# Kernel optimization log

Hardware: AMD Instinct MI355X
Metric: run time of the kernel (lower is better)

## Reference

```python
import jax, jax.numpy as jnp
import numpy as np

B, T, C, L = 256, 1024, 128, 64
BLANK = C - 1          # tf.compat.v1.nn.ctc_loss uses num_classes-1 as blank
EPS = 1e-7             # keras.backend.epsilon()
NEG = -1e30            # log-space 'zero'
S = 2 * L + 1          # extended label length (blanks interleaved)


def setup_inputs() -> dict:
    key = jax.random.key(0)
    k1, k2 = jax.random.split(key)
    # y_pred are softmax probabilities (the layer takes log(y_pred + eps))
    y_pred = jax.nn.softmax(jax.random.normal(k1, (B, T, C), dtype=jnp.float32), axis=-1)
    # labels in [0, C-2]; blank (C-1) never appears in targets
    y_true = jax.random.randint(k2, (B, L), 0, C - 1, dtype=jnp.int32)
    return {"y_true": y_true, "y_pred": y_pred}


def _ctc_loss(y_true, y_pred):
    logp = jnp.log(y_pred + EPS)                                   # [B,T,C]
    # extended label sequence: blank, l1, blank, l2, ..., blank -> [B,S]
    ext = jnp.full((B, S), BLANK, dtype=jnp.int32).at[:, 1::2].set(y_true)
    # gather per-extended-symbol log-probs: lp_ext[b,t,s] = logp[b,t,ext[b,s]]
    lp_ext = jnp.take_along_axis(logp[:, :, None, :], ext[:, None, :, None], axis=-1)[..., 0]  # [B,T,S]
    lp_ext = jnp.transpose(lp_ext, (1, 0, 2))                      # [T,B,S] time-major for scan
    # skip transition allowed where ext[s] != blank and ext[s] != ext[s-2]
    can_skip = jnp.concatenate(
        [jnp.zeros((B, 2), dtype=bool), (ext[:, 2:] != BLANK) & (ext[:, 2:] != ext[:, :-2])],
        axis=1)                                                    # [B,S]

    def shift(a, n):
        return jnp.concatenate([jnp.full((B, n), NEG, a.dtype), a[:, : S - n]], axis=1)

    # alpha init at t=0: only s=0 (blank) and s=1 (first label) reachable
    alpha0 = (jnp.full((B, S), NEG)
              .at[:, 0].set(lp_ext[0, :, 0])
              .at[:, 1].set(lp_ext[0, :, 1]))

    def step(alpha, lp_t):
        s1 = shift(alpha, 1)
        s2 = jnp.where(can_skip, shift(alpha, 2), NEG)
        m = jnp.maximum(alpha, jnp.maximum(s1, s2))                # stable log-sum-exp of 3 terms
        new = m + jnp.log(jnp.exp(alpha - m) + jnp.exp(s1 - m) + jnp.exp(s2 - m)) + lp_t
        return new, None

    alphaT, _ = jax.lax.scan(step, alpha0, lp_ext[1:])
    log_lik = jnp.logaddexp(alphaT[:, -1], alphaT[:, -2])          # end in last blank or last label
    return (-log_lik)[:, None]                                     # [B,1], matches expand_dims(..., 1)


def reference(y_true, y_pred):
    return _ctc_loss(y_true, y_pred)
```

## Files before the change

### kernel.cpp

```cpp
#include <hip/hip_runtime.h>


#define B_     256
#define T_     1024
#define C_     128
#define L_     64
#define BLANK_ 127
#define LN2_   0.69314718055994530942f
#define ROWS   32
#define LDSF   (ROWS * C_)
#define XOFF   (6 * LDSF)

__device__ __forceinline__ float flog2(float x) { return __builtin_amdgcn_logf(x); }

template <int CTRL>
__device__ __forceinline__ int dpp_i(int x) {
    return __builtin_amdgcn_update_dpp(x, x, CTRL, 0xF, 0xF, false);
}
__device__ __forceinline__ float ror1_f(float x) {
    return __int_as_float(dpp_i<0x13C>(__float_as_int(x)));
}
__device__ __forceinline__ int ror1_i(int x) { return dpp_i<0x13C>(x); }

__device__ __forceinline__ float fldexp(float x, int n) {
#if __has_builtin(__builtin_amdgcn_ldexpf)
    return __builtin_amdgcn_ldexpf(x, n);
#else
    return ldexpf(x, n);
#endif
}
__device__ __forceinline__ int fexp_of(float x) {
#if __has_builtin(__builtin_amdgcn_frexp_expf)
    return __builtin_amdgcn_frexp_expf(x);
#else
    const int bx = (__float_as_int(x) >> 23) & 0xFF;
    return (x > 0.0f) ? (bx - 126) : 0;
#endif
}

typedef const __attribute__((address_space(1))) void gas_void;
typedef __attribute__((address_space(3))) void las_void;
__device__ __forceinline__ void g2l16(const float* g, float* l) {
    __builtin_amdgcn_global_load_lds((gas_void*)g, (las_void*)l, 16, 0, 0);
}

#define ALSTEP(pL, pB)                                                        \
    {                                                                         \
        const int   ep  = ror1_i(e);                                          \
        const float mpO = ror1_f(aO);                                         \
        const bool dead = (fmaxf(aE, aO) == 0.0f);                            \
        e = dead ? ep : e;                                                    \
        const int   dd  = ep - e;                                             \
        float prevO = fldexp(mpO, dd);                                        \
        prevO = isL0 ? 0.0f : prevO;                                          \
        const float sk = can_skip ? prevO : 0.0f;                             \
        const float nE = (aE + prevO) * (pB);                                 \
        const float nO = (aO + aE + sk) * (pL);                               \
        aZ = (aZ + aO) * (pB);                                                \
        aE = nE; aO = nO;                                                     \
    }

#define RENORM4                                                               \
    {                                                                         \
        const int x = fexp_of(fmaxf(aE, aO));                                 \
        aE = fldexp(aE, -x); aO = fldexp(aO, -x); aZ = fldexp(aZ, -x);        \
        e += x;                                                               \
    }

#define DCALC                                                                 \
    {                                                                         \
        const int ep = ror1_i(e);                                             \
        d = isL0 ? (-16384) : (ep - e);                                       \
    }

#define RENORM4B { RENORM4 DCALC }

#define BLSTEP(pL, pB)                                                        \
    {                                                                         \
        const float prevO = fldexp(ror1_f(aO), d);                            \
        const float nE = (aE + prevO) * (pB);                                 \
        const float nO = __builtin_fmaf(skf, prevO, aO + aE) * (pL);          \
        aZ = (aZ + aO) * (pB);                                                \
        aE = nE; aO = nO;                                                     \
    }

#define ACHUNK(RL, RB)                                                        \
    {                                                                         \
        _Pragma("unroll")                                                     \
        for (int k = 0; k < 32; ++k) {                                        \
            ALSTEP(RL[k], RB[k])                                              \
            if ((k & 3) == 3) RENORM4                                         \
        }                                                                     \
    }

#define BCHUNK32(RL, RB)                                                      \
    {                                                                         \
        _Pragma("unroll")                                                     \
        for (int k = 0; k < 32; ++k) {                                        \
            BLSTEP(RL[k], RB[k])                                              \
            if ((k & 3) == 3) RENORM4B                                        \
        }                                                                     \
    }

#define STAGE16(ROW, LOFF)                                                    \
    {                                                                         \
        const float* src = base + (size_t)(ROW) * C_;                         \
        _Pragma("unroll")                                                     \
        for (int j = 0; j < 16; ++j)                                          \
            g2l16(src + j * 256 + lane * 4, sm + (LOFF) + j * 256);           \
    }

#define FBURSTM(LOFF, RL, RB)                                                 \
    {                                                                         \
        const float* pl = &sm[(LOFF) + lab];                                  \
        const float* pb = &sm[(LOFF) + BLANK_];                               \
        _Pragma("unroll")                                                     \
        for (int j = 0; j < 32; ++j) RL[j] = pl[j * C_];                      \
        _Pragma("unroll")                                                     \
        for (int j = 0; j < 32; ++j) RB[j] = pb[j * C_];                      \
    }
#define RBURSTM(LOFF, RL, RB)                                                 \
    {                                                                         \
        const float* pl = &sm[(LOFF) + lab];                                  \
        const float* pb = &sm[(LOFF) + BLANK_];                               \
        _Pragma("unroll")                                                     \
        for (int j = 0; j < 32; ++j) RL[j] = pl[(31 - j) * C_];               \
        _Pragma("unroll")                                                     \
        for (int j = 0; j < 32; ++j) RB[j] = pb[(31 - j) * C_];               \
    }

#define VMWAIT asm volatile("s_waitcnt vmcnt(0)" ::: "memory")

#define RUN_HALF(SB, CHUNKROW, BURSTM)                                        \
    {                                                                         \
        float rl0[32], rb0[32], rl1[32], rb1[32];                             \
        STAGE16(CHUNKROW(0), (SB))                                            \
        STAGE16(CHUNKROW(1), (SB) + LDSF)                                     \
        aE = isL0 ? ibase[BLANK_] : 0.0f;                                     \
        aO = isL0 ? ibase[lab]    : 0.0f;                                     \
        VMWAIT;                                                               \
        BURSTM((SB), rl0, rb0)                                   \
        STAGE16(CHUNKROW(2), (SB) + 2 * LDSF)                                 \
        BURSTM((SB) + LDSF, rl1, rb1)                            \
        ACHUNK(rl0, rb0)                                                      \
        VMWAIT;                                                               \
        STAGE16(CHUNKROW(3), (SB))                                            \
        BURSTM((SB) + 2 * LDSF, rl0, rb0)                        \
        ACHUNK(rl1, rb1)                                                      \
        VMWAIT;                                                               \
        STAGE16(CHUNKROW(4), (SB) + LDSF)                                     \
        BURSTM((SB), rl1, rb1)                                   \
        ACHUNK(rl0, rb0)                                                      \
        VMWAIT;                                                               \
        STAGE16(CHUNKROW(5), (SB) + 2 * LDSF)                                 \
        BURSTM((SB) + LDSF, rl0, rb0)                            \
        ACHUNK(rl1, rb1)                                                      \
        VMWAIT;                                                               \
        DCALC                                                                 \
        _Pragma("unroll 1")                                                   \
        for (int c = 4; c <= 12; c += 2) {                                    \
            STAGE16(CHUNKROW(c + 2), (SB) + ((c + 2) % 3) * LDSF)             \
            BURSTM((SB) + ((c + 1) % 3) * LDSF, rl1, rb1)                     \
            BCHUNK32(rl0, rb0)                                                \
            VMWAIT;                                                           \
            STAGE16(CHUNKROW(c + 3), (SB) + ((c + 3) % 3) * LDSF)             \
            BURSTM((SB) + ((c + 2) % 3) * LDSF, rl0, rb0)                     \
            BCHUNK32(rl1, rb1)                                                \
            VMWAIT;                                                           \
        }                                                                     \
        BURSTM((SB), rl1, rb1)                          \
        BCHUNK32(rl0, rb0)                                      \
        _Pragma("unroll")                                                     \
        for (int k = 0; k < 31; ++k) {                \
            BLSTEP(rl1[k], rb1[k])                                            \
            if ((k & 3) == 3) RENORM4B                                        \
        }                                                                     \
    }

#define FROW(k) (1 + 32 * (k))
#define RROW(k) (991 - 32 * (k))

#define ACCP(t, Et)                                                           \
    {                                                                         \
        const float t_ = (t); const int Et_ = (Et);                           \
        const int Em = (Eacc > Et_) ? Eacc : Et_;                             \
        acc = fldexp(acc, Eacc - Em) + fldexp(t_, Et_ - Em);                  \
        Eacc = Em;                                                            \
    }

__global__ __launch_bounds__(128, 1)
void ctc_fwd(const int* __restrict__ yt, const float* __restrict__ yp,
             float* __restrict__ out) {
    __shared__ float sm[6 * LDSF + 320];

    const int b    = blockIdx.x;
    const int tid  = threadIdx.x;
    const int wid  = tid >> 6;
    const int lane = tid & 63;
    const int lidx = (wid == 0) ? lane : (63 - lane);
    const int lab  = yt[b * L_ + lidx];
    const int labp = __shfl_up(lab, 1);
    const bool can_skip = (lane > 0) && (lab != labp);
    const bool isL0     = (lane == 0);
    const bool isL63    = (lane == 63);
    const float skf     = can_skip ? 1.0f : 0.0f;

    const float* __restrict__ base  = yp + (size_t)b * T_ * C_;
    const float* __restrict__ ibase = (wid == 0) ? base : (base + 1023 * C_);

    float aE = 0.0f, aO = 0.0f, aZ = 0.0f;
    int   e  = 0, d = 0;

    if (wid == 0) {
        RUN_HALF(0, FROW, FBURSTM)
    } else {
        RUN_HALF(3 * LDSF, RROW, RBURSTM)
        sm[XOFF + lane]        = aE;
        sm[XOFF + 64 + lane]   = aO;
        sm[XOFF + 128 + lane]  = __int_as_float(e);
        sm[XOFF + 192 + lane]  = aZ;
    }

    __syncthreads();

    if (wid == 0) {
        const int i = lane;
        const float rE_hi = isL0 ? sm[XOFF + 192 + 63] : sm[XOFF + 64 - i];
        const int   e_hi  = __float_as_int(isL0 ? sm[XOFF + 128 + 63]
                                                : sm[XOFF + 128 + 64 - i]);
        const float rO_hi = sm[XOFF + 64 + 63 - i];
        const int   eo_hi = __float_as_int(sm[XOFF + 128 + 63 - i]);
        const float rE_nx = isL63 ? sm[XOFF] : sm[XOFF + 63 - i];
        const int   e_nx  = __float_as_int(isL63 ? sm[XOFF + 128]
                                                 : sm[XOFF + 128 + 63 - i]);
        const float rO_nx = isL63 ? 0.0f : sm[XOFF + 64 + 62 - i];
        const int   eo_nx = isL63 ? 0 : __float_as_int(sm[XOFF + 128 + 62 - i]);
        const int   labn  = __shfl_down(lab, 1);
        const float sknE  = (!isL63 && labn != lab) ? 1.0f : 0.0f;

        float acc = aE * rE_hi;
        int  Eacc = e + e_hi;
        ACCP((aE + aO) * rO_hi, e + eo_hi)
        ACCP((isL63 ? (aO + aZ) : aO) * rE_nx, e + e_nx)
        ACCP(sknE * (aO * rO_nx), e + eo_nx)
        if (acc == 0.0f) Eacc = -(1 << 29);

#pragma unroll
        for (int off = 1; off < 64; off <<= 1) {
            const float s2 = __shfl_xor(acc, off);
            const int   E2 = __shfl_xor(Eacc, off);
            const int   Em = (Eacc > E2) ? Eacc : E2;
            acc = fldexp(acc, Eacc - Em) + fldexp(s2, E2 - Em);
            Eacc = Em;
        }
        if (tid == 0) out[b] = -(flog2(acc) + (float)Eacc) * LN2_;
    }
}

extern "C" void kernel_launch(void* const* d_in, const int* in_sizes, int n_in,
                              void* d_out, int out_size, void* d_ws, size_t ws_size,
                              hipStream_t stream) {
    const int*   y_true = (const int*)d_in[0];
    const float* y_pred = (const float*)d_in[1];
    float*       out    = (float*)d_out;
    ctc_fwd<<<B_, 128, 0, stream>>>(y_true, y_pred, out);
}
```

Baseline: 195.5 us.

## Split forward/backward halves into separate single-wave blocks with a meet kernel

```diff
diff --git a/kernel.cpp b/kernel.cpp
--- a/kernel.cpp
+++ b/kernel.cpp
@@ -9,7 +9,6 @@
 #define LN2_   0.69314718055994530942f
 #define ROWS   32
 #define LDSF   (ROWS * C_)
-#define XOFF   (6 * LDSF)
 
 __device__ __forceinline__ float flog2(float x) { return __builtin_amdgcn_logf(x); }
 
@@ -131,44 +130,44 @@
 
 #define VMWAIT asm volatile("s_waitcnt vmcnt(0)" ::: "memory")
 
-#define RUN_HALF(SB, CHUNKROW, BURSTM)                                        \
+#define RUN_HALF(CHUNKROW, BURSTM)                                            \
     {                                                                         \
         float rl0[32], rb0[32], rl1[32], rb1[32];                             \
-        STAGE16(CHUNKROW(0), (SB))                                            \
-        STAGE16(CHUNKROW(1), (SB) + LDSF)                                     \
+        STAGE16(CHUNKROW(0), 0)                                               \
+        STAGE16(CHUNKROW(1), LDSF)                                            \
         aE = isL0 ? ibase[BLANK_] : 0.0f;                                     \
         aO = isL0 ? ibase[lab]    : 0.0f;                                     \
         VMWAIT;                                                               \
-        BURSTM((SB), rl0, rb0)                                   \
-        STAGE16(CHUNKROW(2), (SB) + 2 * LDSF)                                 \
-        BURSTM((SB) + LDSF, rl1, rb1)                            \
+        BURSTM(0, rl0, rb0)                                      \
+        STAGE16(CHUNKROW(2), 2 * LDSF)                                        \
+        BURSTM(LDSF, rl1, rb1)                                   \
         ACHUNK(rl0, rb0)                                                      \
         VMWAIT;                                                               \
-        STAGE16(CHUNKROW(3), (SB))                                            \
-        BURSTM((SB) + 2 * LDSF, rl0, rb0)                        \
+        STAGE16(CHUNKROW(3), 0)                                               \
+        BURSTM(2 * LDSF, rl0, rb0)                               \
         ACHUNK(rl1, rb1)                                                      \
         VMWAIT;                                                               \
-        STAGE16(CHUNKROW(4), (SB) + LDSF)                                     \
-        BURSTM((SB), rl1, rb1)                                   \
+        STAGE16(CHUNKROW(4), LDSF)                                            \
+        BURSTM(0, rl1, rb1)                                      \
         ACHUNK(rl0, rb0)                                                      \
         VMWAIT;                                                               \
-        STAGE16(CHUNKROW(5), (SB) + 2 * LDSF)                                 \
-        BURSTM((SB) + LDSF, rl0, rb0)                            \
+        STAGE16(CHUNKROW(5), 2 * LDSF)                                        \
+        BURSTM(LDSF, rl0, rb0)                                   \
         ACHUNK(rl1, rb1)                                                      \
         VMWAIT;                                                               \
         DCALC                                                                 \
         _Pragma("unroll 1")                                                   \
         for (int c = 4; c <= 12; c += 2) {                                    \
-            STAGE16(CHUNKROW(c + 2), (SB) + ((c + 2) % 3) * LDSF)             \
-            BURSTM((SB) + ((c + 1) % 3) * LDSF, rl1, rb1)                     \
+            STAGE16(CHUNKROW(c + 2), ((c + 2) % 3) * LDSF)                    \
+            BURSTM(((c + 1) % 3) * LDSF, rl1, rb1)                            \
             BCHUNK32(rl0, rb0)                                                \
             VMWAIT;                                                           \
-            STAGE16(CHUNKROW(c + 3), (SB) + ((c + 3) % 3) * LDSF)             \
-            BURSTM((SB) + ((c + 2) % 3) * LDSF, rl0, rb0)                     \
+            STAGE16(CHUNKROW(c + 3), ((c + 3) % 3) * LDSF)                    \
+            BURSTM(((c + 2) % 3) * LDSF, rl0, rb0)                            \
             BCHUNK32(rl1, rb1)                                                \
             VMWAIT;                                                           \
         }                                                                     \
-        BURSTM((SB), rl1, rb1)                          \
+        BURSTM(0, rl1, rb1)                             \
         BCHUNK32(rl0, rb0)                                      \
         _Pragma("unroll")                                                     \
         for (int k = 0; k < 31; ++k) {                \
@@ -188,73 +187,87 @@
         Eacc = Em;                                                            \
     }
 
-__global__ __launch_bounds__(128, 1)
-void ctc_fwd(const int* __restrict__ yt, const float* __restrict__ yp,
-             float* __restrict__ out) {
-    __shared__ float sm[6 * LDSF + 320];
-
-    const int b    = blockIdx.x;
-    const int tid  = threadIdx.x;
-    const int wid  = tid >> 6;
-    const int lane = tid & 63;
-    const int lidx = (wid == 0) ? lane : (63 - lane);
+__global__ __launch_bounds__(64, 1)
+void ctc_halves(const int* __restrict__ yt, const float* __restrict__ yp,
+                float* __restrict__ ws) {
+    __shared__ float sm[3 * LDSF];
+
+    const int bid  = blockIdx.x;
+    const int b    = bid >> 1;
+    const int dir  = bid & 1;
+    const int lane = threadIdx.x;
+    const int lidx = dir ? (63 - lane) : lane;
     const int lab  = yt[b * L_ + lidx];
     const int labp = __shfl_up(lab, 1);
     const bool can_skip = (lane > 0) && (lab != labp);
     const bool isL0     = (lane == 0);
-    const bool isL63    = (lane == 63);
     const float skf     = can_skip ? 1.0f : 0.0f;
 
     const float* __restrict__ base  = yp + (size_t)b * T_ * C_;
-    const float* __restrict__ ibase = (wid == 0) ? base : (base + 1023 * C_);
+    const float* __restrict__ ibase = dir ? (base + 1023 * C_) : base;
 
     float aE = 0.0f, aO = 0.0f, aZ = 0.0f;
     int   e  = 0, d = 0;
 
-    if (wid == 0) {
-        RUN_HALF(0, FROW, FBURSTM)
+    if (dir == 0) {
+        RUN_HALF(FROW, FBURSTM)
     } else {
-        RUN_HALF(3 * LDSF, RROW, RBURSTM)
-        sm[XOFF + lane]        = aE;
-        sm[XOFF + 64 + lane]   = aO;
-        sm[XOFF + 128 + lane]  = __int_as_float(e);
-        sm[XOFF + 192 + lane]  = aZ;
-    }
-
-    __syncthreads();
-
-    if (wid == 0) {
-        const int i = lane;
-        const float rE_hi = isL0 ? sm[XOFF + 192 + 63] : sm[XOFF + 64 - i];
-        const int   e_hi  = __float_as_int(isL0 ? sm[XOFF + 128 + 63]
-                                                : sm[XOFF + 128 + 64 - i]);
-        const float rO_hi = sm[XOFF + 64 + 63 - i];
-        const int   eo_hi = __float_as_int(sm[XOFF + 128 + 63 - i]);
-        const float rE_nx = isL63 ? sm[XOFF] : sm[XOFF + 63 - i];
-        const int   e_nx  = __float_as_int(isL63 ? sm[XOFF + 128]
-                                                 : sm[XOFF + 128 + 63 - i]);
-        const float rO_nx = isL63 ? 0.0f : sm[XOFF + 64 + 62 - i];
-        const int   eo_nx = isL63 ? 0 : __float_as_int(sm[XOFF + 128 + 62 - i]);
-        const int   labn  = __shfl_down(lab, 1);
-        const float sknE  = (!isL63 && labn != lab) ? 1.0f : 0.0f;
-
-        float acc = aE * rE_hi;
-        int  Eacc = e + e_hi;
-        ACCP((aE + aO) * rO_hi, e + eo_hi)
-        ACCP((isL63 ? (aO + aZ) : aO) * rE_nx, e + e_nx)
-        ACCP(sknE * (aO * rO_nx), e + eo_nx)
-        if (acc == 0.0f) Eacc = -(1 << 29);
+        RUN_HALF(RROW, RBURSTM)
+    }
+
+    float* w4 = ws + (size_t)bid * 256;
+    w4[lane]        = aE;
+    w4[64 + lane]   = aO;
+    w4[128 + lane]  = __int_as_float(e);
+    w4[192 + lane]  = aZ;
+}
+
+__global__ __launch_bounds__(64, 1)
+void ctc_meet(const int* __restrict__ yt, const float* __restrict__ ws,
+              float* __restrict__ out) {
+    const int b    = blockIdx.x;
+    const int lane = threadIdx.x;
+    const int i    = lane;
+    const bool isL0  = (lane == 0);
+    const bool isL63 = (lane == 63);
+
+    const float* wf = ws + (size_t)(2 * b) * 256;
+    const float* wr = wf + 256;
+
+    const float aE = wf[lane];
+    const float aO = wf[64 + lane];
+    const int   e  = __float_as_int(wf[128 + lane]);
+    const float aZ = wf[192 + lane];
+
+    const int lab  = yt[b * L_ + lane];
+    const int labn = __shfl_down(lab, 1);
+    const float sknE = (!isL63 && labn != lab) ? 1.0f : 0.0f;
+
+    const float rE_hi = isL0 ? wr[192 + 63] : wr[64 - i];
+    const int   e_hi  = __float_as_int(isL0 ? wr[128 + 63] : wr[128 + 64 - i]);
+    const float rO_hi = wr[64 + 63 - i];
+    const int   eo_hi = __float_as_int(wr[128 + 63 - i]);
+    const float rE_nx = isL63 ? wr[0] : wr[63 - i];
+    const int   e_nx  = __float_as_int(isL63 ? wr[128] : wr[128 + 63 - i]);
+    const float rO_nx = isL63 ? 0.0f : wr[64 + 62 - i];
+    const int   eo_nx = isL63 ? 0 : __float_as_int(wr[128 + 62 - i]);
+
+    float acc = aE * rE_hi;
+    int  Eacc = e + e_hi;
+    ACCP((aE + aO) * rO_hi, e + eo_hi)
+    ACCP((isL63 ? (aO + aZ) : aO) * rE_nx, e + e_nx)
+    ACCP(sknE * (aO * rO_nx), e + eo_nx)
+    if (acc == 0.0f) Eacc = -(1 << 29);
 
 #pragma unroll
-        for (int off = 1; off < 64; off <<= 1) {
-            const float s2 = __shfl_xor(acc, off);
-            const int   E2 = __shfl_xor(Eacc, off);
-            const int   Em = (Eacc > E2) ? Eacc : E2;
-            acc = fldexp(acc, Eacc - Em) + fldexp(s2, E2 - Em);
-            Eacc = Em;
-        }
-        if (tid == 0) out[b] = -(flog2(acc) + (float)Eacc) * LN2_;
-    }
+    for (int off = 1; off < 64; off <<= 1) {
+        const float s2 = __shfl_xor(acc, off);
+        const int   E2 = __shfl_xor(Eacc, off);
+        const int   Em = (Eacc > E2) ? Eacc : E2;
+        acc = fldexp(acc, Eacc - Em) + fldexp(s2, E2 - Em);
+        Eacc = Em;
+    }
+    if (lane == 0) out[b] = -(flog2(acc) + (float)Eacc) * LN2_;
 }
 
 extern "C" void kernel_launch(void* const* d_in, const int* in_sizes, int n_in,
@@ -263,5 +276,7 @@
     const int*   y_true = (const int*)d_in[0];
     const float* y_pred = (const float*)d_in[1];
     float*       out    = (float*)d_out;
-    ctc_fwd<<<B_, 128, 0, stream>>>(y_true, y_pred, out);
-}
+    float*       ws     = (float*)d_ws;
+    ctc_halves<<<2 * B_, 64, 0, stream>>>(y_true, y_pred, ws);
+    ctc_meet<<<B_, 64, 0, stream>>>(y_true, ws, out);
+}
```

Measured after the change: 198.3 us. Within noise of the previous version (+1.4%).
